# Kernel optimization log

Measured on AMD Instinct MI355X. Metric: run time of the kernel, lower is better.

## Reference

```python
import jax, jax.numpy as jnp
import numpy as np

C = 256        # out_ch / block dim
WS = 16        # window_size
HEADS = 4
HD = C // HEADS
MB = 128       # memory_blocks
LOW = C // 8   # down_rank = 8
SHIFTS = (0, 8, 0, 8)  # depth=4, shift_size = 0 if i%2==0 else 8
WF = 0.1       # weight_factor
EPS = 1e-5


def _rel_pos_index(ws):
    coords = np.stack(np.meshgrid(np.arange(ws), np.arange(ws), indexing="ij")).reshape(2, -1)
    rel = (coords[:, :, None] - coords[:, None, :]).transpose(1, 2, 0) + ws - 1
    return jnp.asarray(rel[..., 0] * (2 * ws - 1) + rel[..., 1])  # [N,N] int


def _shift_mask(H, W, ws, shift):
    # standard Swin shifted-window attention mask, computed statically
    img = np.zeros((H, W))
    cnt = 0
    sls = (slice(0, -ws), slice(-ws, -shift), slice(-shift, None))
    for hs in sls:
        for wss in sls:
            img[hs, wss] = cnt
            cnt += 1
    win = img.reshape(H // ws, ws, W // ws, ws).transpose(0, 2, 1, 3).reshape(-1, ws * ws)
    diff = win[:, None, :] - win[:, :, None]
    return jnp.asarray(np.where(diff != 0, -100.0, 0.0).astype(np.float32))  # [nW,N,N]


def _ln(x, g, b):
    mu = x.mean(-1, keepdims=True)
    var = ((x - mu) ** 2).mean(-1, keepdims=True)
    return (x - mu) * jax.lax.rsqrt(var + EPS) * g + b


def setup_inputs() -> dict:
    key = jax.random.key(0)
    ks = jax.random.split(key, 16)
    B, IN_CH, H, W, D = 8, 64, 64, 64, 4
    w = lambda k, shape: jax.random.normal(k, shape, jnp.float32) * 0.02
    return {
        "x": jax.random.normal(ks[0], (B, IN_CH, H, W), jnp.float32),
        "conv_w": w(ks[1], (C, IN_CH, 3, 3)),
        "bn_gamma": jnp.ones((C,), jnp.float32),
        "bn_beta": jnp.zeros((C,), jnp.float32),
        "bn_mean": jnp.zeros((C,), jnp.float32),
        "bn_var": jnp.ones((C,), jnp.float32),
        "ln1_g": jnp.ones((D, C), jnp.float32),
        "ln1_b": jnp.zeros((D, C), jnp.float32),
        "qkv_w": w(ks[2], (D, 3 * C, C)),
        "qkv_b": jnp.zeros((D, 3 * C), jnp.float32),
        "proj_w": w(ks[3], (D, C, C)),
        "proj_b": jnp.zeros((D, C), jnp.float32),
        "rpb": w(ks[4], (D, (2 * WS - 1) ** 2, HEADS)),
        "mem_bank": w(ks[5], (D, MB, LOW)),
        "down_w": w(ks[6], (D, LOW, C)),
        "down_b": jnp.zeros((D, LOW), jnp.float32),
        "up_w": w(ks[7], (D, C, LOW)),
        "up_b": jnp.zeros((D, C), jnp.float32),
        "ln2_g": jnp.ones((D, C), jnp.float32),
        "ln2_b": jnp.zeros((D, C), jnp.float32),
        "mlp_w1": w(ks[8], (D, 2 * C, C)),
        "mlp_b1": jnp.zeros((D, 2 * C), jnp.float32),
        "mlp_w2": w(ks[9], (D, C, 2 * C)),
        "mlp_b2": jnp.zeros((D, C), jnp.float32),
    }


def reference(x, conv_w, bn_gamma, bn_beta, bn_mean, bn_var, ln1_g, ln1_b,
              qkv_w, qkv_b, proj_w, proj_b, rpb, mem_bank, down_w, down_b,
              up_w, up_b, ln2_g, ln2_b, mlp_w1, mlp_b1, mlp_w2, mlp_b2):
    # conv 3x3 + BN (inference form) + ReLU stem
    y = jax.lax.conv_general_dilated(x, conv_w, (1, 1), ((1, 1), (1, 1)),
                                     dimension_numbers=("NCHW", "OIHW", "NCHW"))
    s = bn_gamma * jax.lax.rsqrt(bn_var + EPS)
    y = jax.nn.relu(y * s[None, :, None, None] + (bn_beta - bn_mean * s)[None, :, None, None])

    B, _, H, W = y.shape
    nH, nW_ = H // WS, W // WS
    nWin, N = nH * nW_, WS * WS
    rpi = _rel_pos_index(WS)
    t = jnp.transpose(y, (0, 2, 3, 1))  # [B,H,W,C]

    for i, shift in enumerate(SHIFTS):
        short = t
        z = _ln(t, ln1_g[i], ln1_b[i])
        if shift:
            z = jnp.roll(z, (-shift, -shift), axis=(1, 2))
        # window partition -> [B*nWin, N, C]
        win = z.reshape(B, nH, WS, nW_, WS, C).transpose(0, 1, 3, 2, 4, 5).reshape(B * nWin, N, C)
        qkv = win @ qkv_w[i].T + qkv_b[i]
        q, k, v = jnp.split(qkv, 3, axis=-1)
        q = q.reshape(-1, N, HEADS, HD).transpose(0, 2, 1, 3)
        k = k.reshape(-1, N, HEADS, HD).transpose(0, 2, 1, 3)
        v = v.reshape(-1, N, HEADS, HD).transpose(0, 2, 1, 3)
        attn = jnp.einsum("whnd,whmd->whnm", q, k) * (HD ** -0.5)
        attn = attn + rpb[i][rpi].transpose(2, 0, 1)[None]  # relative position bias
        if shift:
            mask = _shift_mask(H, W, WS, shift)  # [nWin,N,N]
            attn = (attn.reshape(B, nWin, HEADS, N, N) + mask[None, :, None]).reshape(B * nWin, HEADS, N, N)
        attn = jax.nn.softmax(attn, axis=-1)
        o = jnp.einsum("whnm,whmd->whnd", attn, v).transpose(0, 2, 1, 3).reshape(-1, N, C)
        # low-rank memory bank cross-attention (memory_blocks=128, down_rank=8)
        lowf = o @ down_w[i].T + down_b[i]                       # [B*nWin,N,LOW]
        a = jax.nn.softmax(lowf @ mem_bank[i].T, axis=-1)        # attend over 128 memory slots
        o = o + WF * ((a @ mem_bank[i]) @ up_w[i].T + up_b[i])
        o = o @ proj_w[i].T + proj_b[i]
        # window reverse
        z = o.reshape(B, nH, nW_, WS, WS, C).transpose(0, 1, 3, 2, 4, 5).reshape(B, H, W, C)
        if shift:
            z = jnp.roll(z, (shift, shift), axis=(1, 2))
        t = short + z  # drop_path is identity in deterministic/eval mode
        h = _ln(t, ln2_g[i], ln2_b[i])
        t = t + (jax.nn.gelu(h @ mlp_w1[i].T + mlp_b1[i]) @ mlp_w2[i].T + mlp_b2[i])
    return jnp.transpose(t, (0, 3, 1, 2))  # [B,C,H,W]
```

## Files before the change

### kernel.cpp

```cpp
#include <hip/hip_runtime.h>

using frag_ab = __attribute__((ext_vector_type(8))) short;
using f4v     = __attribute__((ext_vector_type(4))) float;
using u8v     = __attribute__((ext_vector_type(8))) unsigned short;
using u4v     = __attribute__((ext_vector_type(4))) unsigned short;

__device__ __forceinline__ float b2f(unsigned short u){
  return __uint_as_float(((unsigned int)u) << 16);
}
__device__ __forceinline__ unsigned short f2b(float f){
  unsigned int x = __float_as_uint(f);
  unsigned int r = x + 0x7fffu + ((x >> 16) & 1u);
  return (unsigned short)(r >> 16);
}
__device__ __forceinline__ float hexp2(float x){
#if __has_builtin(__builtin_amdgcn_exp2f)
  return __builtin_amdgcn_exp2f(x);
#else
  return exp2f(x);
#endif
}
__device__ __forceinline__ float hrcp(float x){
#if __has_builtin(__builtin_amdgcn_rcpf)
  return __builtin_amdgcn_rcpf(x);
#else
  return 1.0f / x;
#endif
}
__device__ __forceinline__ unsigned int cvtpk(float lo, float hi){
  unsigned int r;
  asm("v_cvt_pk_bf16_f32 %0, %1, %2" : "=v"(r) : "v"(lo), "v"(hi));
  return r;
}
__device__ __forceinline__ void gl16(const void* g, void* l){
  __builtin_amdgcn_global_load_lds(
      (const __attribute__((address_space(1))) unsigned int*)g,
      (__attribute__((address_space(3))) unsigned int*)l, 16, 0, 0);
}

#define MFMA_BF16 __builtin_amdgcn_mfma_f32_16x16x32_bf16

static constexpr size_t OFF_T   = 0;
static constexpr size_t OFF_R1  = 33554432ull;
static constexpr size_t OFF_V   = OFF_R1 + 37748736ull;
static constexpr size_t OFF_VT  = OFF_V + 16777216ull;
static constexpr size_t OFF_ZH  = OFF_VT + 16777216ull;
static constexpr size_t OFF_A   = OFF_ZH + 16777216ull;
static constexpr size_t OFF_WB  = OFF_A + 8388608ull;
static constexpr size_t WB_CONVW = 0;
static constexpr size_t WB_QKVW  = 294912;
static constexpr size_t WB_PROJW = 1867776;
static constexpr size_t WB_MLP1W = 2392064;
static constexpr size_t WB_MLP2W = 3440640;
static constexpr size_t WB_W1    = 4489216;
static constexpr size_t WB_W2T   = 4751360;
static constexpr size_t WB_BLOG  = 5013504;
static constexpr size_t WB_CS    = 5015552;
static constexpr size_t WB_CSH   = 5016576;
static constexpr size_t WB_BIASP = 5017600;

__global__ __launch_bounds__(256) void prep_k(
    const float* __restrict__ conv_w, const float* __restrict__ bn_g, const float* __restrict__ bn_b,
    const float* __restrict__ bn_m, const float* __restrict__ bn_v,
    const float* __restrict__ qkv_w, const float* __restrict__ proj_w,
    const float* __restrict__ mlp_w1, const float* __restrict__ mlp_w2,
    const float* __restrict__ mem_b, const float* __restrict__ down_w, const float* __restrict__ down_b,
    const float* __restrict__ up_w, const float* __restrict__ rpb,
    unsigned short* convwb, unsigned short* qkvwb, unsigned short* projwb,
    unsigned short* mlp1wb, unsigned short* mlp2wb, unsigned short* W1b, unsigned short* W2Tb,
    unsigned short* biasPb, float* blogf, float* convS, float* convSh)
{
  int idx = blockIdx.x * 256 + threadIdx.x;
  if (idx < 256){
    float s = bn_g[idx] * rsqrtf(bn_v[idx] + 1e-5f);
    convS[idx] = s; convSh[idx] = bn_b[idx] - bn_m[idx] * s; return;
  }
  idx -= 256;
  if (idx < 147456){
    int co = idx / 576, kk = idx % 576;
    int t9 = kk >> 6, ci = kk & 63, ky = t9 / 3, kx = t9 % 3;
    convwb[idx] = f2b(conv_w[((co*64 + ci)*3 + ky)*3 + kx]); return;
  }
  idx -= 147456;
  if (idx < 786432){ qkvwb[idx] = f2b(qkv_w[idx]); return; }
  idx -= 786432;
  if (idx < 262144){ projwb[idx] = f2b(proj_w[idx]); return; }
  idx -= 262144;
  if (idx < 524288){ mlp1wb[idx] = f2b(mlp_w1[idx]); return; }
  idx -= 524288;
  if (idx < 524288){ mlp2wb[idx] = f2b(mlp_w2[idx]); return; }
  idx -= 524288;
  if (idx < 131072){
    int i = idx >> 15, rem = idx & 32767, s = rem >> 8, c = rem & 255;
    float acc = 0.f;
    for (int j = 0; j < 32; ++j) acc += mem_b[(i*128 + s)*32 + j] * down_w[(i*32 + j)*256 + c];
    W1b[idx] = f2b(acc * 1.44269504f); return;
  }
  idx -= 131072;
  if (idx < 131072){
    int i = idx >> 15, rem = idx & 32767, c = rem >> 7, s = rem & 127;
    float acc = 0.f;
    for (int j = 0; j < 32; ++j) acc += mem_b[(i*128 + s)*32 + j] * up_w[(i*256 + c)*32 + j];
    W2Tb[idx] = f2b(acc); return;
  }
  idx -= 131072;
  if (idx < 512){
    int i = idx >> 7, s = idx & 127;
    float acc = 0.f;
    for (int j = 0; j < 32; ++j) acc += mem_b[(i*128 + s)*32 + j] * down_b[i*32 + j];
    blogf[idx] = acc * 1.44269504f; return;
  }
  idx -= 512;
  if (idx < 2621440){
    int t = idx >> 18, h = (idx >> 16) & 3, rest = idx & 65535;
    int qb = rest >> 12, kb = (rest >> 8) & 15, q15 = (rest >> 4) & 15, cm = rest & 15;
    int layer, var;
    if (t == 0){ layer = 0; var = 0; }
    else if (t <= 4){ layer = 1; var = t - 1; }
    else if (t == 5){ layer = 2; var = 0; }
    else { layer = 3; var = t - 6; }
    int rn = qb, cn = q15, rm = kb, cm15 = cm;
    int ri = (rn - rm + 15)*31 + (cn - cm15 + 15);
    float b = rpb[((size_t)layer*961 + ri)*4 + h];
    bool mk = ((var & 2) && ((rn < 8) != (rm < 8))) || ((var & 1) && ((cn < 8) != (cm15 < 8)));
    if (mk) b -= 100.0f;
    biasPb[idx] = f2b(b * 1.44269504f);
  }
}

__global__ __launch_bounds__(256) void pad_k(const float* __restrict__ x, unsigned short* __restrict__ xp)
{
  const int bid = blockIdx.x;
  const int b = bid / 66, hp = bid % 66;
  const int tid = threadIdx.x;
  unsigned short* orow = xp + ((size_t)(b*66 + hp))*66*64;
  const u8v Z8 = {0,0,0,0,0,0,0,0};
  if (hp == 0 || hp == 65){
    for (int s = tid; s < 528; s += 256) *(u8v*)&orow[s*8] = Z8;
    return;
  }
  __shared__ float ls[64][65];
  const int h = hp - 1;
  {
    int cc = tid >> 2, w4 = (tid & 3)*16;
    const float* src = &x[((size_t)(b*64 + cc)*64 + h)*64 + w4];
    #pragma unroll
    for (int j = 0; j < 4; ++j){
      float4 v = *(const float4*)&src[j*4];
      ls[w4 + j*4 + 0][cc] = v.x; ls[w4 + j*4 + 1][cc] = v.y;
      ls[w4 + j*4 + 2][cc] = v.z; ls[w4 + j*4 + 3][cc] = v.w;
    }
  }
  __syncthreads();
  if (tid < 16){
    int wp = (tid >> 3) * 65;
    *(u8v*)&orow[(size_t)wp*64 + (tid & 7)*8] = Z8;
  }
  int w = tid >> 2, c0 = (tid & 3)*16;
  u8v o0, o1;
  #pragma unroll
  for (int e = 0; e < 8; ++e){ o0[e] = f2b(ls[w][c0+e]); o1[e] = f2b(ls[w][c0+8+e]); }
  *(u8v*)&orow[(size_t)(w+1)*64 + c0] = o0;
  *(u8v*)&orow[(size_t)(w+1)*64 + c0 + 8] = o1;
}

struct Ep {
  const float* c0; const float* c1;
  const float* lg; const float* lb;
  float* t;
  unsigned short* o0; unsigned short* o2;
  unsigned short* q; unsigned short* k; unsigned short* v;
  const unsigned short* in0;
  int shift;
};
enum { M_CONV=0, M_QKV=1, M_MEM1S=2, M_MEM2=3, M_PROJLN=4, M_MLP1=5, M_MLP2LN=6 };

template<int MODE, int TM, int TN, int KC>
__global__ __launch_bounds__(512) void g512_k(const unsigned short* __restrict__ X,
                                              const unsigned short* __restrict__ W, Ep ep)
{
  __shared__ __align__(16) unsigned short Als[2][TM*32];
  __shared__ __align__(16) unsigned short Bls[2][TN*32];
  const int tid = threadIdx.x, wid = tid >> 6, lane = tid & 63, g = lane >> 4, l15 = lane & 15;
  constexpr int NW = TN/64;
  const int wr = wid / NW, wc = wid % NW;
  const int row0 = blockIdx.x * TM, col0 = blockIdx.y * TN;
  constexpr int KT = KC >> 5;
  constexpr int NA = TM/128, NB = TN/128;

  const unsigned short* gA[NA]; int rbA[NA];
  #pragma unroll
  for (int i = 0; i < NA; ++i){
    int s = tid + 512*i, r = s >> 2, p = s & 3, lb = p ^ ((r >> 1) & 3);
    if constexpr (MODE == M_CONV){
      int ar = row0 + r, bi = ar >> 12, h = (ar >> 6) & 63, w = ar & 63;
      rbA[i] = ((bi*66 + h + 1)*66 + (w + 1))*64 + lb*8; gA[i] = nullptr;
    } else { gA[i] = &X[(size_t)(row0 + r)*KC + lb*8]; rbA[i] = 0; }
  }
  const unsigned short* gB[NB];
  #pragma unroll
  for (int i = 0; i < NB; ++i){
    int s = tid + 512*i, r = s >> 2, p = s & 3, lb = p ^ ((r >> 1) & 3);
    gB[i] = &W[(size_t)(col0 + r)*KC + lb*8];
  }

  f4v acc[4][4] = {};

  auto stage = [&](int kt, int buf){
    #pragma unroll
    for (int i = 0; i < NA; ++i){
      if constexpr (MODE == M_CONV){
        int t9 = kt >> 1, ky = t9 / 3, kx = t9 - ky*3;
        int koff = ((ky - 1)*66 + (kx - 1))*64 + (kt & 1)*32;
        gl16(X + rbA[i] + koff, &Als[buf][(tid + 512*i)*8]);
      } else {
        gl16(gA[i] + kt*32, &Als[buf][(tid + 512*i)*8]);
      }
    }
    #pragma unroll
    for (int i = 0; i < NB; ++i) gl16(gB[i] + kt*32, &Bls[buf][(tid + 512*i)*8]);
  };
  auto compute = [&](const unsigned short* A, const unsigned short* B){
    frag_ab af[4], bv[4];
    #pragma unroll
    for (int a = 0; a < 4; ++a){ int r = wr*64 + a*16 + l15; int pb = g ^ ((r >> 1) & 3);
      af[a] = *(const frag_ab*)&A[r*32 + pb*8]; }
    #pragma unroll
    for (int b = 0; b < 4; ++b){ int r = wc*64 + b*16 + l15; int pb = g ^ ((r >> 1) & 3);
      bv[b] = *(const frag_ab*)&B[r*32 + pb*8]; }
    #pragma unroll
    for (int a = 0; a < 4; ++a)
      #pragma unroll
      for (int b = 0; b < 4; ++b)
        acc[a][b] = MFMA_BF16(af[a], bv[b], acc[a][b], 0, 0, 0);
  };

  stage(0, 0);
  __syncthreads();
  for (int kt = 0; kt < KT; kt += 2){
    stage(kt + 1, 1);
    compute(Als[0], Bls[0]);
    __syncthreads();
    if (kt + 2 < KT) stage(kt + 2, 0);
    compute(Als[1], Bls[1]);
    __syncthreads();
  }

  float* red = (float*)&Als[0][0];

  if constexpr (MODE == M_QKV){
    const int which = col0 >> 8;
    #pragma unroll
    for (int a = 0; a < 4; ++a){
      #pragma unroll
      for (int b = 0; b < 4; ++b){
        const int grow0 = row0 + wr*64 + a*16 + g*4;
        const int hd = b*16 + l15;
        const int bcol = wc*64 + hd;
        const float bv = ep.c0[col0 - (col0 & 255) + bcol];
        if (which == 2){
          int win = grow0 >> 8, tok0 = grow0 & 255;
          int pos = (tok0 & ~31) | ((tok0 & 12) << 1) | ((tok0 & 16) >> 2);
          u4v o;
          #pragma unroll
          for (int r = 0; r < 4; ++r) o[r] = f2b(acc[a][b][r] + bv);
          *(u4v*)&ep.v[(((size_t)((grow0 >> 8)*4 + wc)*64 + hd)*256) + pos] = o;
          (void)win;
        } else {
          unsigned short* dst = (which == 0) ? ep.q : ep.k;
          float sc = (which == 0) ? 0.18033688f : 1.0f;
          #pragma unroll
          for (int r = 0; r < 4; ++r){
            int grow = grow0 + r;
            dst[(((size_t)(grow >> 8)*4 + wc)*256 + (grow & 255))*64 + hd] = f2b((acc[a][b][r] + bv) * sc);
          }
        }
      }
    }
  } else if constexpr (MODE == M_MEM1S){
    #pragma unroll
    for (int a = 0; a < 4; ++a){
      #pragma unroll
      for (int r = 0; r < 4; ++r){
        float s1 = 0.f;
        #pragma unroll
        for (int b = 0; b < 4; ++b){
          int bcol = wc*64 + b*16 + l15;
          float e = hexp2(acc[a][b][r] + ep.c0[bcol]);
          acc[a][b][r] = e; s1 += e;
        }
        s1 += __shfl_xor(s1, 1); s1 += __shfl_xor(s1, 2);
        s1 += __shfl_xor(s1, 4); s1 += __shfl_xor(s1, 8);
        if (l15 == 0){
          int rl = wr*64 + a*16 + g*4 + r;
          red[rl*NW + wc] = s1;
        }
      }
    }
    __syncthreads();
    #pragma unroll
    for (int a = 0; a < 4; ++a){
      #pragma unroll
      for (int r = 0; r < 4; ++r){
        int rl = wr*64 + a*16 + g*4 + r;
        float inv = 1.0f / (red[rl*NW] + red[rl*NW + 1]);
        int grow = row0 + rl;
        #pragma unroll
        for (int b = 0; b < 4; ++b){
          int bcol = wc*64 + b*16 + l15;
          ep.o0[(size_t)grow*128 + bcol] = f2b(acc[a][b][r] * inv);
        }
      }
    }
  } else if constexpr (MODE == M_MEM2){
    #pragma unroll
    for (int a = 0; a < 4; ++a)
      #pragma unroll
      for (int b = 0; b < 4; ++b)
        #pragma unroll
        for (int r = 0; r < 4; ++r){
          int grow = row0 + wr*64 + a*16 + g*4 + r;
          int bcol = wc*64 + b*16 + l15;
          size_t ix = (size_t)grow*256 + bcol;
          ep.o0[ix] = f2b(b2f(ep.in0[ix]) + 0.1f*(acc[a][b][r] + ep.c0[bcol]));
        }
  } else if constexpr (MODE == M_MLP1){
    #pragma unroll
    for (int a = 0; a < 4; ++a)
      #pragma unroll
      for (int b = 0; b < 4; ++b)
        #pragma unroll
        for (int r = 0; r < 4; ++r){
          int grow = row0 + wr*64 + a*16 + g*4 + r;
          int gcol = col0 + wc*64 + b*16 + l15;
          float xq = acc[a][b][r] + ep.c0[gcol];
          float x3 = xq*xq*xq;
          float e = hexp2(xq*2.3022115f + x3*0.10294856f);
          float gl = xq - xq*hrcp(e + 1.0f);
          ep.o0[(size_t)grow*512 + gcol] = f2b(gl);
        }
  } else {
    #pragma unroll
    for (int a = 0; a < 4; ++a){
      #pragma unroll
      for (int r = 0; r < 4; ++r){
        const int grow = row0 + wr*64 + a*16 + g*4 + r;
        int srow;
        if constexpr (MODE == M_PROJLN){
          int win = grow >> 8, tok = grow & 255;
          int bb = win >> 4, whh = (win >> 2) & 3, www = win & 3, rr = tok >> 4, cc = tok & 15;
          srow = (bb*64 + ((whh*16 + rr + ep.shift) & 63))*64 + ((www*16 + cc + ep.shift) & 63);
        } else srow = grow;
        float s1 = 0.f, s2 = 0.f;
        #pragma unroll
        for (int b = 0; b < 4; ++b){
          int bcol = wc*64 + b*16 + l15;
          float v = acc[a][b][r];
          if constexpr (MODE == M_CONV) v = fmaxf(v*ep.c0[bcol] + ep.c1[bcol], 0.f);
          else v = ep.t[(size_t)srow*256 + bcol] + v + ep.c0[bcol];
          acc[a][b][r] = v;
          ep.t[(size_t)srow*256 + bcol] = v;
          s1 += v; s2 += v*v;
        }
        s1 += __shfl_xor(s1, 1); s2 += __shfl_xor(s2, 1);
        s1 += __shfl_xor(s1, 2); s2 += __shfl_xor(s2, 2);
        s1 += __shfl_xor(s1, 4); s2 += __shfl_xor(s2, 4);
        s1 += __shfl_xor(s1, 8); s2 += __shfl_xor(s2, 8);
        if (l15 == 0){
          int rl = wr*64 + a*16 + g*4 + r;
          red[rl*8 + wc*2]     = s1;
          red[rl*8 + wc*2 + 1] = s2;
        }
      }
    }
    __syncthreads();
    if (MODE != M_MLP2LN || ep.o2 != nullptr){
      #pragma unroll
      for (int a = 0; a < 4; ++a){
        #pragma unroll
        for (int r = 0; r < 4; ++r){
          const int grow = row0 + wr*64 + a*16 + g*4 + r;
          int rl = wr*64 + a*16 + g*4 + r;
          float s1 = red[rl*8] + red[rl*8+2] + red[rl*8+4] + red[rl*8+6];
          float s2 = red[rl*8+1] + red[rl*8+3] + red[rl*8+5] + red[rl*8+7];
          float mu = s1 * (1.0f/256.0f);
          float var = s2 * (1.0f/256.0f) - mu*mu;
          float rstd = rsqrtf(var + 1e-5f);
          int drow;
          unsigned short* zo;
          if constexpr (MODE == M_PROJLN){ drow = 0; zo = ep.o0; }
          else { zo = (MODE == M_MLP2LN) ? ep.o2 : ep.o0; drow = 0; }
          if constexpr (MODE == M_PROJLN){
            int win = grow >> 8, tok = grow & 255;
            int bb = win >> 4, whh = (win >> 2) & 3, www = win & 3, rr = tok >> 4, cc = tok & 15;
            drow = (bb*64 + ((whh*16 + rr + ep.shift) & 63))*64 + ((www*16 + cc + ep.shift) & 63);
          } else {
            int bb2 = grow >> 12, h = (grow >> 6) & 63, w = grow & 63;
            int hs = (h - ep.shift) & 63, ws = (w - ep.shift) & 63;
            drow = (bb2*16 + (hs >> 4)*4 + (ws >> 4))*256 + (hs & 15)*16 + (ws & 15);
          }
          #pragma unroll
          for (int b = 0; b < 4; ++b){
            int bcol = wc*64 + b*16 + l15;
            float v = acc[a][b][r];
            zo[(size_t)drow*256 + bcol] = f2b((v - mu)*rstd*ep.lg[bcol] + ep.lb[bcol]);
          }
        }
      }
    }
  }
}

__global__ __launch_bounds__(512, 4) void attn_k(const unsigned short* __restrict__ qg_,
    const unsigned short* __restrict__ kg_, const unsigned short* __restrict__ vt_,
    const unsigned short* __restrict__ biasP, unsigned short* __restrict__ ob, int shift)
{
  __shared__ __align__(16) unsigned short Kl[16384];
  __shared__ __align__(16) unsigned short Vl[16384];
  const int tid = threadIdx.x, wid = tid >> 6, lane = tid & 63, g = lane >> 4, q15 = lane & 15;
  const int blk = blockIdx.x, win = blk >> 2, head = blk & 3;
  const int wh = (win >> 2) & 3, ww = win & 3;
  const unsigned short* kg = kg_ + (size_t)blk*16384;
  const unsigned short* vg = vt_ + (size_t)blk*16384;
  const unsigned short* qg = qg_ + (size_t)blk*16384;
  const int var = shift ? (((wh == 3) ? 2 : 0) | ((ww == 3) ? 1 : 0)) : 0;
  const unsigned short* bT = biasP + ((size_t)var*4 + head)*65536;

  #pragma unroll
  for (int it = 0; it < 4; ++it){
    int s = it*512 + tid;
    int r = s >> 3, lb = (s & 7) ^ (r & 7);
    gl16(&kg[r*64 + lb*8], &Kl[s*8]);
    int hd = s >> 5, cc = s & 31, cs = (cc & 16) | ((cc & 15) ^ (hd & 15));
    gl16(&vg[hd*256 + cs*8], &Vl[s*8]);
  }
  __syncthreads();

  const f4v Z4 = {0.f, 0.f, 0.f, 0.f};
  for (int c = 0; c < 2; ++c){
    const int nq = wid*32 + c*16 + q15;
    const int qb = wid*2 + c;
    frag_ab qf0 = *(const frag_ab*)&qg[nq*64 + g*8];
    frag_ab qf1 = *(const frag_ab*)&qg[nq*64 + 32 + g*8];
    unsigned int pk[32];
    float vsum = 0.f;
    #pragma unroll
    for (int t2 = 0; t2 < 16; ++t2){
      int r = t2*16 + q15;
      f4v a = Z4;
      { int pb = g ^ (r & 7);
        frag_ab ak = *(const frag_ab*)&Kl[r*64 + pb*8];
        a = MFMA_BF16(ak, qf0, a, 0, 0, 0); }
      { int pb = (4 + g) ^ (r & 7);
        frag_ab ak = *(const frag_ab*)&Kl[r*64 + pb*8];
        a = MFMA_BF16(ak, qf1, a, 0, 0, 0); }
      u4v bb = *(const u4v*)&bT[((qb*16 + t2)*16 + q15)*16 + g*4];
      float p0 = hexp2(a[0] + b2f(bb[0]));
      float p1 = hexp2(a[1] + b2f(bb[1]));
      float p2 = hexp2(a[2] + b2f(bb[2]));
      float p3 = hexp2(a[3] + b2f(bb[3]));
      vsum += (p0 + p1) + (p2 + p3);
      pk[2*t2]   = cvtpk(p0, p1);
      pk[2*t2+1] = cvtpk(p2, p3);
    }
    vsum += __shfl_xor(vsum, 16);
    vsum += __shfl_xor(vsum, 32);
    float inv = 1.0f / vsum;
    float invl[4];
    #pragma unroll
    for (int r = 0; r < 4; ++r) invl[r] = __shfl(inv, g*4 + r);
    f4v oc[4];
    #pragma unroll
    for (int nn = 0; nn < 4; ++nn) oc[nn] = Z4;
    __builtin_amdgcn_s_setprio(1);
    #pragma unroll
    for (int s = 0; s < 8; ++s){
      union { frag_ab f; unsigned int u[4]; } pa;
      pa.u[0] = pk[4*s + 0];
      pa.u[1] = pk[4*s + 1];
      pa.u[2] = pk[4*s + 2];
      pa.u[3] = pk[4*s + 3];
      #pragma unroll
      for (int nn = 0; nn < 4; ++nn){
        int hd = nn*16 + q15;
        int cc = s*4 + g;
        int cs = (cc & 16) | ((cc & 15) ^ (hd & 15));
        frag_ab bv = *(const frag_ab*)&Vl[hd*256 + cs*8];
        oc[nn] = MFMA_BF16(pa.f, bv, oc[nn], 0, 0, 0);
      }
    }
    __builtin_amdgcn_s_setprio(0);
    #pragma unroll
    for (int nn = 0; nn < 4; ++nn)
      #pragma unroll
      for (int r = 0; r < 4; ++r){
        int qq = wid*32 + c*16 + g*4 + r;
        ob[((size_t)(win*256 + qq))*256 + head*64 + nn*16 + q15] = f2b(oc[nn][r] * invl[r]);
      }
  }
}

__global__ __launch_bounds__(256) void nchw_k(const float* __restrict__ t, float* __restrict__ out)
{
  __shared__ float ls[64*65];
  int bh = blockIdx.x; int b = bh >> 6, h = bh & 63; int tid = threadIdx.x;
  for (int c0 = 0; c0 < 256; c0 += 64){
    #pragma unroll
    for (int rr = 0; rr < 4; ++rr){
      int s = rr*256 + tid;
      int w = s >> 4, c4 = s & 15;
      float4 v = *(const float4*)&t[((size_t)((b*64 + h)*64 + w))*256 + c0 + c4*4];
      ls[w*65 + c4*4 + 0] = v.x; ls[w*65 + c4*4 + 1] = v.y;
      ls[w*65 + c4*4 + 2] = v.z; ls[w*65 + c4*4 + 3] = v.w;
    }
    __syncthreads();
    int c = tid & 63, wq = tid >> 6;
    float buf[16];
    #pragma unroll
    for (int k2 = 0; k2 < 16; ++k2) buf[k2] = ls[(wq*16 + k2)*65 + c];
    size_t obase = ((size_t)(b*256 + c0 + c))*4096 + h*64 + wq*16;
    #pragma unroll
    for (int k2 = 0; k2 < 16; k2 += 4){
      float4 o4 = make_float4(buf[k2], buf[k2+1], buf[k2+2], buf[k2+3]);
      *(float4*)&out[obase + k2] = o4;
    }
    __syncthreads();
  }
}

extern "C" void kernel_launch(void* const* d_in, const int* in_sizes, int n_in,
                              void* d_out, int out_size, void* d_ws, size_t ws_size,
                              hipStream_t stream)
{
  (void)in_sizes; (void)n_in; (void)out_size; (void)ws_size;
  const float* x      = (const float*)d_in[0];
  const float* conv_w = (const float*)d_in[1];
  const float* bn_g   = (const float*)d_in[2];
  const float* bn_b   = (const float*)d_in[3];
  const float* bn_m   = (const float*)d_in[4];
  const float* bn_v   = (const float*)d_in[5];
  const float* ln1_g  = (const float*)d_in[6];
  const float* ln1_b  = (const float*)d_in[7];
  const float* qkv_w  = (const float*)d_in[8];
  const float* qkv_b  = (const float*)d_in[9];
  const float* proj_w = (const float*)d_in[10];
  const float* proj_b = (const float*)d_in[11];
  const float* rpb    = (const float*)d_in[12];
  const float* mem_b  = (const float*)d_in[13];
  const float* down_w = (const float*)d_in[14];
  const float* down_b = (const float*)d_in[15];
  const float* up_w   = (const float*)d_in[16];
  const float* up_b   = (const float*)d_in[17];
  const float* ln2_g  = (const float*)d_in[18];
  const float* ln2_b  = (const float*)d_in[19];
  const float* mlp_w1 = (const float*)d_in[20];
  const float* mlp_b1 = (const float*)d_in[21];
  const float* mlp_w2 = (const float*)d_in[22];
  const float* mlp_b2 = (const float*)d_in[23];

  char* ws = (char*)d_ws;
  float*          tbuf  = (float*)(ws + OFF_T);
  unsigned short* xpb   = (unsigned short*)(ws + OFF_R1);
  unsigned short* qbuf  = (unsigned short*)(ws + OFF_R1);
  unsigned short* kbuf  = (unsigned short*)(ws + OFF_R1 + 16777216ull);
  unsigned short* gbuf  = (unsigned short*)(ws + OFF_R1);
  unsigned short* o2buf = (unsigned short*)(ws + OFF_V);
  unsigned short* vtbuf = (unsigned short*)(ws + OFF_VT);
  unsigned short* zbuf  = (unsigned short*)(ws + OFF_ZH);
  unsigned short* abuf  = (unsigned short*)(ws + OFF_A);
  unsigned short* convwb = (unsigned short*)(ws + OFF_WB + WB_CONVW);
  unsigned short* qkvwb  = (unsigned short*)(ws + OFF_WB + WB_QKVW);
  unsigned short* projwb = (unsigned short*)(ws + OFF_WB + WB_PROJW);
  unsigned short* mlp1wb = (unsigned short*)(ws + OFF_WB + WB_MLP1W);
  unsigned short* mlp2wb = (unsigned short*)(ws + OFF_WB + WB_MLP2W);
  unsigned short* W1b    = (unsigned short*)(ws + OFF_WB + WB_W1);
  unsigned short* W2Tb   = (unsigned short*)(ws + OFF_WB + WB_W2T);
  float*          blogf  = (float*)(ws + OFF_WB + WB_BLOG);
  float*          convS  = (float*)(ws + OFF_WB + WB_CS);
  float*          convSh = (float*)(ws + OFF_WB + WB_CSH);
  unsigned short* biasPb = (unsigned short*)(ws + OFF_WB + WB_BIASP);

  prep_k<<<20036, 256, 0, stream>>>(conv_w, bn_g, bn_b, bn_m, bn_v, qkv_w, proj_w, mlp_w1, mlp_w2,
                                    mem_b, down_w, down_b, up_w, rpb,
                                    convwb, qkvwb, projwb, mlp1wb, mlp2wb, W1b, W2Tb, biasPb,
                                    blogf, convS, convSh);
  pad_k<<<528, 256, 0, stream>>>(x, xpb);
  { Ep ep{convS, convSh, ln1_g, ln1_b, tbuf, zbuf, nullptr, nullptr, nullptr, nullptr, nullptr, 0};
    g512_k<M_CONV,128,256,576><<<dim3(256,1), 512, 0, stream>>>(xpb, convwb, ep); }

  static const int tb[4] = {0, 1, 5, 6};
  for (int i = 0; i < 4; ++i){
    int shift = (i & 1) ? 8 : 0;
    int shift_next = (i < 3) ? (((i + 1) & 1) ? 8 : 0) : 0;
    { Ep ep{qkv_b + i*768, nullptr, nullptr, nullptr, nullptr, nullptr, nullptr, qbuf, kbuf, vtbuf, nullptr, 0};
      g512_k<M_QKV,128,256,256><<<dim3(256,3), 512, 0, stream>>>(zbuf, qkvwb + (size_t)i*196608, ep); }
    attn_k<<<512, 512, 0, stream>>>(qbuf, kbuf, vtbuf, biasPb + (size_t)tb[i]*262144, zbuf, shift);
    { Ep ep{blogf + i*128, nullptr, nullptr, nullptr, nullptr, abuf, nullptr, nullptr, nullptr, nullptr, nullptr, 0};
      g512_k<M_MEM1S,256,128,256><<<dim3(128,1), 512, 0, stream>>>(zbuf, W1b + (size_t)i*32768, ep); }
    { Ep ep{up_b + i*256, nullptr, nullptr, nullptr, nullptr, o2buf, nullptr, nullptr, nullptr, nullptr, zbuf, 0};
      g512_k<M_MEM2,128,256,128><<<dim3(256,1), 512, 0, stream>>>(abuf, W2Tb + (size_t)i*32768, ep); }
    { Ep ep{proj_b + i*256, nullptr, ln2_g + i*256, ln2_b + i*256, tbuf, zbuf, nullptr, nullptr, nullptr, nullptr, nullptr, shift};
      g512_k<M_PROJLN,128,256,256><<<dim3(256,1), 512, 0, stream>>>(o2buf, projwb + (size_t)i*65536, ep); }
    { Ep ep{mlp_b1 + i*512, nullptr, nullptr, nullptr, nullptr, gbuf, nullptr, nullptr, nullptr, nullptr, nullptr, 0};
      g512_k<M_MLP1,128,256,256><<<dim3(256,2), 512, 0, stream>>>(zbuf, mlp1wb + (size_t)i*131072, ep); }
    { unsigned short* znext = (i < 3) ? zbuf : nullptr;
      const float* lg = (i < 3) ? (ln1_g + (i+1)*256) : ln1_g;
      const float* lb = (i < 3) ? (ln1_b + (i+1)*256) : ln1_b;
      Ep ep{mlp_b2 + i*256, nullptr, lg, lb, tbuf, nullptr, znext, nullptr, nullptr, nullptr, nullptr, shift_next};
      g512_k<M_MLP2LN,128,256,512><<<dim3(256,1), 512, 0, stream>>>(gbuf, mlp2wb + (size_t)i*131072, ep); }
  }
  nchw_k<<<512, 256, 0, stream>>>(tbuf, (float*)d_out);
}
```

Before: 761.0 us.

## Fold memory-bank up-projection into proj GEMM and fuse final NCHW output

```diff
diff --git a/kernel.cpp b/kernel.cpp
--- a/kernel.cpp
+++ b/kernel.cpp
@@ -58,6 +58,8 @@
 static constexpr size_t WB_CS    = 5015552;
 static constexpr size_t WB_CSH   = 5016576;
 static constexpr size_t WB_BIASP = 5017600;
+static constexpr size_t WB_PW2   = WB_BIASP + 5242880;
+static constexpr size_t WB_PB2   = WB_PW2 + 786432;
 
 __global__ __launch_bounds__(256) void prep_k(
     const float* __restrict__ conv_w, const float* __restrict__ bn_g, const float* __restrict__ bn_b,
@@ -119,12 +121,37 @@
     else if (t <= 4){ layer = 1; var = t - 1; }
     else if (t == 5){ layer = 2; var = 0; }
     else { layer = 3; var = t - 6; }
-    int rn = qb, cn = q15, rm = kb, cm15 = cm;
-    int ri = (rn - rm + 15)*31 + (cn - cm15 + 15);
+    int ri = (qb - kb + 15)*31 + (q15 - cm + 15);
     float b = rpb[((size_t)layer*961 + ri)*4 + h];
-    bool mk = ((var & 2) && ((rn < 8) != (rm < 8))) || ((var & 1) && ((cn < 8) != (cm15 < 8)));
+    bool mk = ((var & 2) && ((qb < 8) != (kb < 8))) || ((var & 1) && ((q15 < 8) != (cm < 8)));
     if (mk) b -= 100.0f;
     biasPb[idx] = f2b(b * 1.44269504f);
+  }
+}
+
+__global__ __launch_bounds__(256) void prep2_k(const float* __restrict__ proj_w,
+    const float* __restrict__ up_b, const float* __restrict__ proj_b,
+    const unsigned short* __restrict__ W2Tb, unsigned short* __restrict__ pw2, float* __restrict__ pb2)
+{
+  int idx = blockIdx.x * 256 + threadIdx.x;
+  if (idx < 1024){
+    int i = idx >> 8, o = idx & 255;
+    float acc = proj_b[i*256 + o];
+    for (int c = 0; c < 256; ++c) acc += 0.1f * up_b[i*256 + c] * proj_w[((size_t)(i*256 + o))*256 + c];
+    pb2[idx] = acc; return;
+  }
+  idx -= 1024;
+  if (idx < 262144){
+    int i = idx >> 16, rem = idx & 65535, o = rem >> 8, c = rem & 255;
+    pw2[((size_t)(i*256 + o))*384 + c] = f2b(proj_w[((size_t)(i*256 + o))*256 + c]); return;
+  }
+  idx -= 262144;
+  if (idx < 131072){
+    int i = idx >> 15, rem = idx & 32767, o = rem >> 7, s = rem & 127;
+    float acc = 0.f;
+    for (int c = 0; c < 256; ++c)
+      acc += proj_w[((size_t)(i*256 + o))*256 + c] * b2f(W2Tb[(i*256 + c)*128 + s]);
+    pw2[((size_t)(i*256 + o))*384 + 256 + s] = f2b(0.1f * acc);
   }
 }
 
@@ -167,17 +194,17 @@
 struct Ep {
   const float* c0; const float* c1;
   const float* lg; const float* lb;
-  float* t;
+  float* t; float* outp;
   unsigned short* o0; unsigned short* o2;
   unsigned short* q; unsigned short* k; unsigned short* v;
   const unsigned short* in0;
   int shift;
 };
-enum { M_CONV=0, M_QKV=1, M_MEM1S=2, M_MEM2=3, M_PROJLN=4, M_MLP1=5, M_MLP2LN=6 };
-
-template<int MODE, int TM, int TN, int KC>
-__global__ __launch_bounds__(512) void g512_k(const unsigned short* __restrict__ X,
-                                              const unsigned short* __restrict__ W, Ep ep)
+enum { M_CONV=0, M_QKV=1, M_MEM1S=2, M_PROJLN=3, M_MLP1=4, M_MLP2LN=5, M_MLP2OUT=6 };
+
+template<int MODE, int TM, int TN, int KC, int NT>
+__global__ __launch_bounds__(NT) void g512_k(const unsigned short* __restrict__ X,
+                                             const unsigned short* __restrict__ W, Ep ep)
 {
   __shared__ __align__(16) unsigned short Als[2][TM*32];
   __shared__ __align__(16) unsigned short Bls[2][TN*32];
@@ -186,21 +213,26 @@
   const int wr = wid / NW, wc = wid % NW;
   const int row0 = blockIdx.x * TM, col0 = blockIdx.y * TN;
   constexpr int KT = KC >> 5;
-  constexpr int NA = TM/128, NB = TN/128;
-
-  const unsigned short* gA[NA]; int rbA[NA];
+  constexpr int NA = (TM*4)/NT, NB = (TN*4)/NT;
+
+  const unsigned short* gA[NA]; const unsigned short* gA2[NA]; int rbA[NA];
   #pragma unroll
   for (int i = 0; i < NA; ++i){
-    int s = tid + 512*i, r = s >> 2, p = s & 3, lb = p ^ ((r >> 1) & 3);
+    int s = tid + NT*i, r = s >> 2, p = s & 3, lb = p ^ ((r >> 1) & 3);
+    gA2[i] = nullptr;
     if constexpr (MODE == M_CONV){
       int ar = row0 + r, bi = ar >> 12, h = (ar >> 6) & 63, w = ar & 63;
       rbA[i] = ((bi*66 + h + 1)*66 + (w + 1))*64 + lb*8; gA[i] = nullptr;
-    } else { gA[i] = &X[(size_t)(row0 + r)*KC + lb*8]; rbA[i] = 0; }
+    } else {
+      constexpr int KA = (MODE == M_PROJLN) ? 256 : KC;
+      gA[i] = &X[(size_t)(row0 + r)*KA + lb*8]; rbA[i] = 0;
+      if constexpr (MODE == M_PROJLN) gA2[i] = &ep.in0[(size_t)(row0 + r)*128 + lb*8];
+    }
   }
   const unsigned short* gB[NB];
   #pragma unroll
   for (int i = 0; i < NB; ++i){
-    int s = tid + 512*i, r = s >> 2, p = s & 3, lb = p ^ ((r >> 1) & 3);
+    int s = tid + NT*i, r = s >> 2, p = s & 3, lb = p ^ ((r >> 1) & 3);
     gB[i] = &W[(size_t)(col0 + r)*KC + lb*8];
   }
 
@@ -212,13 +244,16 @@
       if constexpr (MODE == M_CONV){
         int t9 = kt >> 1, ky = t9 / 3, kx = t9 - ky*3;
         int koff = ((ky - 1)*66 + (kx - 1))*64 + (kt & 1)*32;
-        gl16(X + rbA[i] + koff, &Als[buf][(tid + 512*i)*8]);
+        gl16(X + rbA[i] + koff, &Als[buf][(tid + NT*i)*8]);
+      } else if constexpr (MODE == M_PROJLN){
+        if (kt < 8) gl16(gA[i] + kt*32, &Als[buf][(tid + NT*i)*8]);
+        else        gl16(gA2[i] + (kt - 8)*32, &Als[buf][(tid + NT*i)*8]);
       } else {
-        gl16(gA[i] + kt*32, &Als[buf][(tid + 512*i)*8]);
-      }
-    }
-    #pragma unroll
-    for (int i = 0; i < NB; ++i) gl16(gB[i] + kt*32, &Bls[buf][(tid + 512*i)*8]);
+        gl16(gA[i] + kt*32, &Als[buf][(tid + NT*i)*8]);
+      }
+    }
+    #pragma unroll
+    for (int i = 0; i < NB; ++i) gl16(gB[i] + kt*32, &Bls[buf][(tid + NT*i)*8]);
   };
   auto compute = [&](const unsigned short* A, const unsigned short* B){
     frag_ab af[4], bv[4];
@@ -256,16 +291,14 @@
       for (int b = 0; b < 4; ++b){
         const int grow0 = row0 + wr*64 + a*16 + g*4;
         const int hd = b*16 + l15;
-        const int bcol = wc*64 + hd;
-        const float bv = ep.c0[col0 - (col0 & 255) + bcol];
+        const float bv = ep.c0[col0 + wc*64 + hd];
         if (which == 2){
-          int win = grow0 >> 8, tok0 = grow0 & 255;
+          int tok0 = grow0 & 255;
           int pos = (tok0 & ~31) | ((tok0 & 12) << 1) | ((tok0 & 16) >> 2);
           u4v o;
           #pragma unroll
           for (int r = 0; r < 4; ++r) o[r] = f2b(acc[a][b][r] + bv);
           *(u4v*)&ep.v[(((size_t)((grow0 >> 8)*4 + wc)*64 + hd)*256) + pos] = o;
-          (void)win;
         } else {
           unsigned short* dst = (which == 0) ? ep.q : ep.k;
           float sc = (which == 0) ? 0.18033688f : 1.0f;
@@ -312,18 +345,6 @@
         }
       }
     }
-  } else if constexpr (MODE == M_MEM2){
-    #pragma unroll
-    for (int a = 0; a < 4; ++a)
-      #pragma unroll
-      for (int b = 0; b < 4; ++b)
-        #pragma unroll
-        for (int r = 0; r < 4; ++r){
-          int grow = row0 + wr*64 + a*16 + g*4 + r;
-          int bcol = wc*64 + b*16 + l15;
-          size_t ix = (size_t)grow*256 + bcol;
-          ep.o0[ix] = f2b(b2f(ep.in0[ix]) + 0.1f*(acc[a][b][r] + ep.c0[bcol]));
-        }
   } else if constexpr (MODE == M_MLP1){
     #pragma unroll
     for (int a = 0; a < 4; ++a)
@@ -339,6 +360,20 @@
           float gl = xq - xq*hrcp(e + 1.0f);
           ep.o0[(size_t)grow*512 + gcol] = f2b(gl);
         }
+  } else if constexpr (MODE == M_MLP2OUT){
+    #pragma unroll
+    for (int a = 0; a < 4; ++a){
+      #pragma unroll
+      for (int b = 0; b < 4; ++b){
+        const int grow0 = row0 + wr*64 + a*16 + g*4;
+        const int bcol = wc*64 + b*16 + l15;
+        float4 vv;
+        #pragma unroll
+        for (int r = 0; r < 4; ++r)
+          (&vv.x)[r] = ep.t[(size_t)(grow0 + r)*256 + bcol] + acc[a][b][r] + ep.c0[bcol];
+        *(float4*)&ep.outp[((size_t)((grow0 >> 12)*256 + bcol))*4096 + (grow0 & 4095)] = vv;
+      }
+    }
   } else {
     #pragma unroll
     for (int a = 0; a < 4; ++a){
@@ -374,37 +409,33 @@
       }
     }
     __syncthreads();
-    if (MODE != M_MLP2LN || ep.o2 != nullptr){
-      #pragma unroll
-      for (int a = 0; a < 4; ++a){
+    #pragma unroll
+    for (int a = 0; a < 4; ++a){
+      #pragma unroll
+      for (int r = 0; r < 4; ++r){
+        const int grow = row0 + wr*64 + a*16 + g*4 + r;
+        int rl = wr*64 + a*16 + g*4 + r;
+        float s1 = red[rl*8] + red[rl*8+2] + red[rl*8+4] + red[rl*8+6];
+        float s2 = red[rl*8+1] + red[rl*8+3] + red[rl*8+5] + red[rl*8+7];
+        float mu = s1 * (1.0f/256.0f);
+        float var = s2 * (1.0f/256.0f) - mu*mu;
+        float rstd = rsqrtf(var + 1e-5f);
+        unsigned short* zo = (MODE == M_MLP2LN) ? ep.o2 : ep.o0;
+        int drow;
+        if constexpr (MODE == M_PROJLN){
+          int win = grow >> 8, tok = grow & 255;
+          int bb = win >> 4, whh = (win >> 2) & 3, www = win & 3, rr = tok >> 4, cc = tok & 15;
+          drow = (bb*64 + ((whh*16 + rr + ep.shift) & 63))*64 + ((www*16 + cc + ep.shift) & 63);
+        } else {
+          int bb2 = grow >> 12, h = (grow >> 6) & 63, w = grow & 63;
+          int hs = (h - ep.shift) & 63, ws = (w - ep.shift) & 63;
+          drow = (bb2*16 + (hs >> 4)*4 + (ws >> 4))*256 + (hs & 15)*16 + (ws & 15);
+        }
         #pragma unroll
-        for (int r = 0; r < 4; ++r){
-          const int grow = row0 + wr*64 + a*16 + g*4 + r;
-          int rl = wr*64 + a*16 + g*4 + r;
-          float s1 = red[rl*8] + red[rl*8+2] + red[rl*8+4] + red[rl*8+6];
-          float s2 = red[rl*8+1] + red[rl*8+3] + red[rl*8+5] + red[rl*8+7];
-          float mu = s1 * (1.0f/256.0f);
-          float var = s2 * (1.0f/256.0f) - mu*mu;
-          float rstd = rsqrtf(var + 1e-5f);
-          int drow;
-          unsigned short* zo;
-          if constexpr (MODE == M_PROJLN){ drow = 0; zo = ep.o0; }
-          else { zo = (MODE == M_MLP2LN) ? ep.o2 : ep.o0; drow = 0; }
-          if constexpr (MODE == M_PROJLN){
-            int win = grow >> 8, tok = grow & 255;
-            int bb = win >> 4, whh = (win >> 2) & 3, www = win & 3, rr = tok >> 4, cc = tok & 15;
-            drow = (bb*64 + ((whh*16 + rr + ep.shift) & 63))*64 + ((www*16 + cc + ep.shift) & 63);
-          } else {
-            int bb2 = grow >> 12, h = (grow >> 6) & 63, w = grow & 63;
-            int hs = (h - ep.shift) & 63, ws = (w - ep.shift) & 63;
-            drow = (bb2*16 + (hs >> 4)*4 + (ws >> 4))*256 + (hs & 15)*16 + (ws & 15);
-          }
-          #pragma unroll
-          for (int b = 0; b < 4; ++b){
-            int bcol = wc*64 + b*16 + l15;
-            float v = acc[a][b][r];
-            zo[(size_t)drow*256 + bcol] = f2b((v - mu)*rstd*ep.lg[bcol] + ep.lb[bcol]);
-          }
+        for (int b = 0; b < 4; ++b){
+          int bcol = wc*64 + b*16 + l15;
+          float v = acc[a][b][r];
+          zo[(size_t)drow*256 + bcol] = f2b((v - mu)*rstd*ep.lg[bcol] + ep.lb[bcol]);
         }
       }
     }
@@ -497,34 +528,6 @@
         int qq = wid*32 + c*16 + g*4 + r;
         ob[((size_t)(win*256 + qq))*256 + head*64 + nn*16 + q15] = f2b(oc[nn][r] * invl[r]);
       }
-  }
-}
-
-__global__ __launch_bounds__(256) void nchw_k(const float* __restrict__ t, float* __restrict__ out)
-{
-  __shared__ float ls[64*65];
-  int bh = blockIdx.x; int b = bh >> 6, h = bh & 63; int tid = threadIdx.x;
-  for (int c0 = 0; c0 < 256; c0 += 64){
-    #pragma unroll
-    for (int rr = 0; rr < 4; ++rr){
-      int s = rr*256 + tid;
-      int w = s >> 4, c4 = s & 15;
-      float4 v = *(const float4*)&t[((size_t)((b*64 + h)*64 + w))*256 + c0 + c4*4];
-      ls[w*65 + c4*4 + 0] = v.x; ls[w*65 + c4*4 + 1] = v.y;
-      ls[w*65 + c4*4 + 2] = v.z; ls[w*65 + c4*4 + 3] = v.w;
-    }
-    __syncthreads();
-    int c = tid & 63, wq = tid >> 6;
-    float buf[16];
-    #pragma unroll
-    for (int k2 = 0; k2 < 16; ++k2) buf[k2] = ls[(wq*16 + k2)*65 + c];
-    size_t obase = ((size_t)(b*256 + c0 + c))*4096 + h*64 + wq*16;
-    #pragma unroll
-    for (int k2 = 0; k2 < 16; k2 += 4){
-      float4 o4 = make_float4(buf[k2], buf[k2+1], buf[k2+2], buf[k2+3]);
-      *(float4*)&out[obase + k2] = o4;
-    }
-    __syncthreads();
   }
 }
 
@@ -564,7 +567,7 @@
   unsigned short* qbuf  = (unsigned short*)(ws + OFF_R1);
   unsigned short* kbuf  = (unsigned short*)(ws + OFF_R1 + 16777216ull);
   unsigned short* gbuf  = (unsigned short*)(ws + OFF_R1);
-  unsigned short* o2buf = (unsigned short*)(ws + OFF_V);
+  unsigned short* hbuf  = (unsigned short*)(ws + OFF_V);
   unsigned short* vtbuf = (unsigned short*)(ws + OFF_VT);
   unsigned short* zbuf  = (unsigned short*)(ws + OFF_ZH);
   unsigned short* abuf  = (unsigned short*)(ws + OFF_A);
@@ -579,35 +582,37 @@
   float*          convS  = (float*)(ws + OFF_WB + WB_CS);
   float*          convSh = (float*)(ws + OFF_WB + WB_CSH);
   unsigned short* biasPb = (unsigned short*)(ws + OFF_WB + WB_BIASP);
+  unsigned short* pw2b   = (unsigned short*)(ws + OFF_WB + WB_PW2);
+  float*          pb2f   = (float*)(ws + OFF_WB + WB_PB2);
 
   prep_k<<<20036, 256, 0, stream>>>(conv_w, bn_g, bn_b, bn_m, bn_v, qkv_w, proj_w, mlp_w1, mlp_w2,
                                     mem_b, down_w, down_b, up_w, rpb,
                                     convwb, qkvwb, projwb, mlp1wb, mlp2wb, W1b, W2Tb, biasPb,
                                     blogf, convS, convSh);
+  prep2_k<<<1540, 256, 0, stream>>>(proj_w, up_b, proj_b, W2Tb, pw2b, pb2f);
   pad_k<<<528, 256, 0, stream>>>(x, xpb);
-  { Ep ep{convS, convSh, ln1_g, ln1_b, tbuf, zbuf, nullptr, nullptr, nullptr, nullptr, nullptr, 0};
-    g512_k<M_CONV,128,256,576><<<dim3(256,1), 512, 0, stream>>>(xpb, convwb, ep); }
+  { Ep ep{convS, convSh, ln1_g, ln1_b, tbuf, nullptr, zbuf, nullptr, nullptr, nullptr, nullptr, nullptr, 0};
+    g512_k<M_CONV,128,256,576,512><<<dim3(256,1), 512, 0, stream>>>(xpb, convwb, ep); }
 
   static const int tb[4] = {0, 1, 5, 6};
   for (int i = 0; i < 4; ++i){
     int shift = (i & 1) ? 8 : 0;
-    int shift_next = (i < 3) ? (((i + 1) & 1) ? 8 : 0) : 0;
-    { Ep ep{qkv_b + i*768, nullptr, nullptr, nullptr, nullptr, nullptr, nullptr, qbuf, kbuf, vtbuf, nullptr, 0};
-      g512_k<M_QKV,128,256,256><<<dim3(256,3), 512, 0, stream>>>(zbuf, qkvwb + (size_t)i*196608, ep); }
+    int shift_next = ((i + 1) & 1) ? 8 : 0;
+    { Ep ep{qkv_b + i*768, nullptr, nullptr, nullptr, nullptr, nullptr, nullptr, nullptr, qbuf, kbuf, vtbuf, nullptr, 0};
+      g512_k<M_QKV,128,256,256,512><<<dim3(256,3), 512, 0, stream>>>(zbuf, qkvwb + (size_t)i*196608, ep); }
     attn_k<<<512, 512, 0, stream>>>(qbuf, kbuf, vtbuf, biasPb + (size_t)tb[i]*262144, zbuf, shift);
-    { Ep ep{blogf + i*128, nullptr, nullptr, nullptr, nullptr, abuf, nullptr, nullptr, nullptr, nullptr, nullptr, 0};
-      g512_k<M_MEM1S,256,128,256><<<dim3(128,1), 512, 0, stream>>>(zbuf, W1b + (size_t)i*32768, ep); }
-    { Ep ep{up_b + i*256, nullptr, nullptr, nullptr, nullptr, o2buf, nullptr, nullptr, nullptr, nullptr, zbuf, 0};
-      g512_k<M_MEM2,128,256,128><<<dim3(256,1), 512, 0, stream>>>(abuf, W2Tb + (size_t)i*32768, ep); }
-    { Ep ep{proj_b + i*256, nullptr, ln2_g + i*256, ln2_b + i*256, tbuf, zbuf, nullptr, nullptr, nullptr, nullptr, nullptr, shift};
-      g512_k<M_PROJLN,128,256,256><<<dim3(256,1), 512, 0, stream>>>(o2buf, projwb + (size_t)i*65536, ep); }
-    { Ep ep{mlp_b1 + i*512, nullptr, nullptr, nullptr, nullptr, gbuf, nullptr, nullptr, nullptr, nullptr, nullptr, 0};
-      g512_k<M_MLP1,128,256,256><<<dim3(256,2), 512, 0, stream>>>(zbuf, mlp1wb + (size_t)i*131072, ep); }
-    { unsigned short* znext = (i < 3) ? zbuf : nullptr;
-      const float* lg = (i < 3) ? (ln1_g + (i+1)*256) : ln1_g;
-      const float* lb = (i < 3) ? (ln1_b + (i+1)*256) : ln1_b;
-      Ep ep{mlp_b2 + i*256, nullptr, lg, lb, tbuf, nullptr, znext, nullptr, nullptr, nullptr, nullptr, shift_next};
-      g512_k<M_MLP2LN,128,256,512><<<dim3(256,1), 512, 0, stream>>>(gbuf, mlp2wb + (size_t)i*131072, ep); }
-  }
-  nchw_k<<<512, 256, 0, stream>>>(tbuf, (float*)d_out);
-}
+    { Ep ep{blogf + i*128, nullptr, nullptr, nullptr, nullptr, nullptr, abuf, nullptr, nullptr, nullptr, nullptr, nullptr, 0};
+      g512_k<M_MEM1S,256,128,256,512><<<dim3(128,1), 512, 0, stream>>>(zbuf, W1b + (size_t)i*32768, ep); }
+    { Ep ep{pb2f + i*256, nullptr, ln2_g + i*256, ln2_b + i*256, tbuf, nullptr, hbuf, nullptr, nullptr, nullptr, nullptr, abuf, shift};
+      g512_k<M_PROJLN,128,256,384,512><<<dim3(256,1), 512, 0, stream>>>(zbuf, pw2b + (size_t)i*98304, ep); }
+    { Ep ep{mlp_b1 + i*512, nullptr, nullptr, nullptr, nullptr, nullptr, gbuf, nullptr, nullptr, nullptr, nullptr, nullptr, 0};
+      g512_k<M_MLP1,128,256,256,512><<<dim3(256,2), 512, 0, stream>>>(hbuf, mlp1wb + (size_t)i*131072, ep); }
+    if (i < 3){
+      Ep ep{mlp_b2 + i*256, nullptr, ln1_g + (i+1)*256, ln1_b + (i+1)*256, tbuf, nullptr, nullptr, zbuf, nullptr, nullptr, nullptr, nullptr, shift_next};
+      g512_k<M_MLP2LN,128,256,512,512><<<dim3(256,1), 512, 0, stream>>>(gbuf, mlp2wb + (size_t)i*131072, ep);
+    } else {
+      Ep ep{mlp_b2 + i*256, nullptr, nullptr, nullptr, tbuf, (float*)d_out, nullptr, nullptr, nullptr, nullptr, nullptr, nullptr, 0};
+      g512_k<M_MLP2OUT,128,256,512,512><<<dim3(256,1), 512, 0, stream>>>(gbuf, mlp2wb + (size_t)i*131072, ep);
+    }
+  }
+}
```

Result: faster. 692.0 us (-9.1%).
